# Optimization experiments

Measured on AMD Instinct MI355X. Metric: run time of the kernel, lower is better.

Reference implementation:

```python
import jax, jax.numpy as jnp
import numpy as np

NUM_GRAPHS = 512
NODES_PER_GRAPH = 200  # == N_rois
EDGES_PER_GRAPH = 3200  # avg degree 16
N_ROIS = 200
HIDDEN = 64
OUT = 2


def setup_inputs() -> dict:
    key = jax.random.key(0)
    ks = jax.random.split(key, 7)
    N = NUM_GRAPHS * NODES_PER_GRAPH
    E = NUM_GRAPHS * EDGES_PER_GRAPH
    x = jax.random.normal(ks[0], (N, N_ROIS), dtype=jnp.float32)
    # edges sampled within each graph's node block
    base = jnp.repeat(jnp.arange(NUM_GRAPHS, dtype=jnp.int64) * NODES_PER_GRAPH, EDGES_PER_GRAPH)
    local = jax.random.randint(ks[1], (2, E), 0, NODES_PER_GRAPH, dtype=jnp.int64)
    edge_index = local + base[None, :]
    batch = jnp.arange(N, dtype=jnp.int64) // NODES_PER_GRAPH
    conv_w = jax.random.normal(ks[2], (N_ROIS, HIDDEN), dtype=jnp.float32) * 0.1
    conv_b = jax.random.normal(ks[3], (HIDDEN,), dtype=jnp.float32) * 0.1
    lin_w = jax.random.normal(ks[4], (HIDDEN, OUT), dtype=jnp.float32) * 0.1
    lin_b = jax.random.normal(ks[5], (OUT,), dtype=jnp.float32) * 0.1
    return {"x": x, "edge_index": edge_index, "batch": batch,
            "conv_w": conv_w, "conv_b": conv_b, "lin_w": lin_w, "lin_b": lin_b}


def reference(x, edge_index, batch, conv_w, conv_b, lin_w, lin_b):
    N = x.shape[0]
    # GCNConv: linear transform first (N_rois -> hidden), then normalized aggregation
    h = x @ conv_w  # [N, H]
    loops = jnp.arange(N, dtype=edge_index.dtype)
    src = jnp.concatenate([edge_index[0], loops])  # add self-loops (PyG default)
    dst = jnp.concatenate([edge_index[1], loops])
    deg = jax.ops.segment_sum(jnp.ones_like(dst, dtype=h.dtype), dst, num_segments=N)
    dinv = jnp.where(deg > 0, jax.lax.rsqrt(deg), jnp.zeros_like(deg))
    norm = dinv[src] * dinv[dst]  # D^-1/2 (A+I) D^-1/2 edge weights
    agg = jax.ops.segment_sum(h[src] * norm[:, None], dst, num_segments=N) + conv_b
    hr = jax.nn.relu(agg)
    x_pool = jax.ops.segment_max(hr, batch, num_segments=NUM_GRAPHS)  # [G, H]
    out = x_pool @ lin_w + lin_b  # [G, OUT]
    return out, x_pool
```

## Files before the change

### kernel.cpp

```cpp
#include <hip/hip_runtime.h>

#define NUM_GRAPHS 512
#define NPG 200
#define EPG 3200
#define NROIS 200
#define HID 64
#define OUTC 2
#define APITCH 232
#define HPITCH 232
#define WIMG_ELEMS (7 * 4 * 2 * 64 * 8)
#define WS_NEEDED ((size_t)WIMG_ELEMS * 2)

typedef short v8s __attribute__((ext_vector_type(8)));
typedef float v4f __attribute__((ext_vector_type(4)));

__device__ __forceinline__ unsigned bf16_rne(float f) {
  unsigned u = __float_as_uint(f);
  return (u + 0x7fffu + ((u >> 16) & 1u)) >> 16;
}

__global__ void prep_wimg(const float* __restrict__ cw, unsigned short* __restrict__ wimg) {
  int idx = blockIdx.x * 256 + threadIdx.x;
  if (idx >= WIMG_ELEMS) return;
  int i    = idx & 7;
  int lane = (idx >> 3) & 63;
  int hl   = (idx >> 9) & 1;
  int nt   = (idx >> 10) & 3;
  int kt   = idx >> 12;
  int k  = kt * 32 + (lane >> 4) * 8 + i;
  int ch = nt * 16 + (lane & 15);
  float f = (k < NROIS) ? cw[k * HID + ch] : 0.f;
  unsigned hi = bf16_rne(f);
  float lo = f - __uint_as_float(hi << 16);
  wimg[idx] = hl ? (unsigned short)(__float_as_uint(lo) >> 16) : (unsigned short)hi;
}

struct __align__(16) Smem2 {
  unsigned char adj[208 * APITCH];
  union {
    unsigned short hpTl[HID * HPITCH];
    unsigned int wbuf[2][2048];
  } u;
  int cnt[NPG];
  float dinv[NPG];
  int pool[HID];
};

__device__ __forceinline__ v8s tobf16(const float4& a, const float4& b) {
  v8s r;
  r[0] = (short)bf16_rne(a.x); r[1] = (short)bf16_rne(a.y);
  r[2] = (short)bf16_rne(a.z); r[3] = (short)bf16_rne(a.w);
  r[4] = (short)bf16_rne(b.x); r[5] = (short)bf16_rne(b.y);
  r[6] = (short)bf16_rne(b.z); r[7] = (short)bf16_rne(b.w);
  return r;
}

__device__ __forceinline__ void stageW(Smem2& s, const unsigned short* __restrict__ wimg,
                                       int kt, int buf, int w, int lane) {
  const char* gp = (const char*)wimg + (size_t)kt * 8192 + (size_t)(w * 64 + lane) * 16;
  unsigned char* lp = (unsigned char*)&s.u.wbuf[buf][0] + w * 1024;
  __builtin_amdgcn_global_load_lds(
      (const __attribute__((address_space(1))) unsigned int*)gp,
      (__attribute__((address_space(3))) unsigned int*)lp, 16, 0, 0);
}

__device__ __forceinline__ void xfetch(const float* __restrict__ x, int base,
                                       int kt, int q, const int* mts, const int* nrow,
                                       float4 xa[2][2]) {
  const int k0 = kt * 32 + q * 8;
  const bool ok = (k0 + 8 <= NROIS);
  #pragma unroll
  for (int mi = 0; mi < 2; ++mi) {
    if (mts[mi] >= 0) {
      if (ok) {
        const float* px = x + (size_t)(base + nrow[mi]) * NROIS + k0;
        xa[mi][0] = *(const float4*)px;
        xa[mi][1] = *(const float4*)(px + 4);
      } else {
        xa[mi][0] = make_float4(0.f, 0.f, 0.f, 0.f);
        xa[mi][1] = make_float4(0.f, 0.f, 0.f, 0.f);
      }
    }
  }
}

__global__ __launch_bounds__(512, 4)
void gcn_fused8(const float* __restrict__ x,
                const int* __restrict__ ei,
                const unsigned short* __restrict__ wimg,
                const float* __restrict__ cb,
                const float* __restrict__ lw,
                const float* __restrict__ lb,
                float* __restrict__ out,
                int Etot) {
  __shared__ Smem2 s;
  const int g = blockIdx.x;
  const int tid = threadIdx.x;
  const int base = g * NPG;
  const int ebase = g * EPG;
  const int lane = tid & 63;
  const int w = __builtin_amdgcn_readfirstlane(tid >> 6);
  const int ml = tid & 15;
  const int q  = (tid >> 4) & 3;

  int mts[2];
  mts[0] = w;
  mts[1] = (w < 5) ? 8 + w : -1;
  int nrow[2];
  #pragma unroll
  for (int mi = 0; mi < 2; ++mi) {
    int node = mts[mi] * 16 + ml;
    nrow[mi] = (node < NPG) ? node : 0;
  }

  int esrc[7], edst[7];
  #pragma unroll
  for (int r = 0; r < 7; ++r) {
    int e = tid + r * 512;
    esrc[r] = -1; edst[r] = 0;
    if (e < EPG) {
      esrc[r] = ei[ebase + e] - base;
      edst[r] = ei[Etot + ebase + e] - base;
    }
  }
  float4 xa[2][2];
  xfetch(x, base, 0, q, mts, nrow, xa);
  stageW(s, wimg, 0, 0, w, lane);
  {
    uint4* z = (uint4*)s.adj;
    const uint4 z4 = {0u, 0u, 0u, 0u};
    #pragma unroll
    for (int i = 0; i < 6; ++i) {
      int idx = tid + i * 512;
      if (idx < (208 * APITCH) / 16) z[idx] = z4;
    }
    if (tid < NPG) s.cnt[tid] = 0;
    if (tid < HID) s.pool[tid] = 0;
  }
  __syncthreads();

  {
    unsigned* adjW = (unsigned*)s.adj;
    #pragma unroll
    for (int r = 0; r < 7; ++r) {
      if (esrc[r] >= 0) {
        int idx = edst[r] * APITCH + esrc[r];
        atomicAdd(&adjW[idx >> 2], 1u << ((idx & 3) * 8));
        atomicAdd(&s.cnt[edst[r]], 1);
      }
    }
    if (tid < NPG) {
      int idx = tid * APITCH + tid;
      atomicAdd(&adjW[idx >> 2], 1u << ((idx & 3) * 8));
    }
  }

  v4f acc[2][4];
  #pragma unroll
  for (int a = 0; a < 2; ++a)
    #pragma unroll
    for (int b = 0; b < 4; ++b)
      acc[a][b] = (v4f){0.f, 0.f, 0.f, 0.f};

  for (int kt = 0; kt < 7; ++kt) {
    const int cur = kt & 1;
    if (kt < 6) stageW(s, wimg, kt + 1, cur ^ 1, w, lane);
    v8s xh2[2];
    #pragma unroll
    for (int mi = 0; mi < 2; ++mi)
      if (mts[mi] >= 0) xh2[mi] = tobf16(xa[mi][0], xa[mi][1]);
    if (kt < 6) xfetch(x, base, kt + 1, q, mts, nrow, xa);

    const unsigned short* wb = (const unsigned short*)&s.u.wbuf[cur][0];
    v8s whi[4], wlo[4];
    #pragma unroll
    for (int nt = 0; nt < 4; ++nt) {
      whi[nt] = *(const v8s*)(wb + (size_t)((nt * 2 + 0) * 64 + lane) * 8);
      wlo[nt] = *(const v8s*)(wb + (size_t)((nt * 2 + 1) * 64 + lane) * 8);
    }
    #pragma unroll
    for (int mi = 0; mi < 2; ++mi) {
      if (mts[mi] >= 0) {
        #pragma unroll
        for (int nt = 0; nt < 4; ++nt) {
          acc[mi][nt] = __builtin_amdgcn_mfma_f32_16x16x32_bf16(wlo[nt], xh2[mi], acc[mi][nt], 0, 0, 0);
          acc[mi][nt] = __builtin_amdgcn_mfma_f32_16x16x32_bf16(whi[nt], xh2[mi], acc[mi][nt], 0, 0, 0);
        }
      }
    }
    __syncthreads();
  }

  if (tid < NPG) s.dinv[tid] = rsqrtf((float)(s.cnt[tid] + 1));
  {
    int ch = tid >> 3, grp = tid & 7;
    *(uint2*)&s.u.hpTl[ch * HPITCH + 200 + grp * 4] = (uint2){0u, 0u};
  }
  #pragma unroll
  for (int mi = 0; mi < 2; ++mi) {
    if (mts[mi] >= 0) {
      const int node = mts[mi] * 16 + ml;
      if (node < NPG) {
        const float dv = rsqrtf((float)(s.cnt[node] + 1));
        #pragma unroll
        for (int nt = 0; nt < 4; ++nt) {
          #pragma unroll
          for (int r = 0; r < 4; ++r) {
            const int ch = nt * 16 + q * 4 + r;
            s.u.hpTl[ch * HPITCH + node] = (unsigned short)bf16_rne(dv * acc[mi][nt][r]);
          }
        }
      }
    }
  }
  __syncthreads();

  {
    v4f acc2[2][4];
    #pragma unroll
    for (int a = 0; a < 2; ++a)
      #pragma unroll
      for (int b = 0; b < 4; ++b)
        acc2[a][b] = (v4f){0.f, 0.f, 0.f, 0.f};

    for (int kt = 0; kt < 7; ++kt) {
      const int k0 = kt * 32 + q * 8;

      v8s bf[4];
      #pragma unroll
      for (int nt = 0; nt < 4; ++nt)
        bf[nt] = *(const v8s*)&s.u.hpTl[(nt * 16 + ml) * HPITCH + k0];

      #pragma unroll
      for (int mi = 0; mi < 2; ++mi) {
        if (mts[mi] >= 0) {
          const int row = mts[mi] * 16 + ml;
          const uint2 dd = *(const uint2*)&s.adj[row * APITCH + k0];
          v8s af;
          #pragma unroll
          for (int i = 0; i < 4; ++i) {
            af[i]     = (short)(__float_as_uint((float)((dd.x >> (8 * i)) & 0xffu)) >> 16);
            af[i + 4] = (short)(__float_as_uint((float)((dd.y >> (8 * i)) & 0xffu)) >> 16);
          }
          #pragma unroll
          for (int nt = 0; nt < 4; ++nt)
            acc2[mi][nt] = __builtin_amdgcn_mfma_f32_16x16x32_bf16(af, bf[nt], acc2[mi][nt], 0, 0, 0);
        }
      }
    }

    float cbv[4];
    #pragma unroll
    for (int nt = 0; nt < 4; ++nt) cbv[nt] = cb[nt * 16 + ml];
    float mx[4] = {0.f, 0.f, 0.f, 0.f};
    #pragma unroll
    for (int mi = 0; mi < 2; ++mi) {
      if (mts[mi] >= 0) {
        #pragma unroll
        for (int r = 0; r < 4; ++r) {
          const int row = mts[mi] * 16 + q * 4 + r;
          if (row < NPG) {
            const float dv = s.dinv[row];
            #pragma unroll
            for (int nt = 0; nt < 4; ++nt) {
              float v = fmaxf(fmaf(dv, acc2[mi][nt][r], cbv[nt]), 0.f);
              mx[nt] = fmaxf(mx[nt], v);
            }
          }
        }
      }
    }
    #pragma unroll
    for (int nt = 0; nt < 4; ++nt) {
      mx[nt] = fmaxf(mx[nt], __shfl_xor(mx[nt], 16));
      mx[nt] = fmaxf(mx[nt], __shfl_xor(mx[nt], 32));
    }
    if (q == 0 && (lane >> 5) == 0) {
      #pragma unroll
      for (int nt = 0; nt < 4; ++nt)
        atomicMax(&s.pool[nt * 16 + ml], __float_as_int(mx[nt]));
    }
  }
  __syncthreads();

  if (tid < HID) {
    const float xp = __int_as_float(s.pool[tid]);
    out[NUM_GRAPHS * OUTC + g * HID + tid] = xp;
    float p0 = xp * lw[tid * 2 + 0];
    float p1 = xp * lw[tid * 2 + 1];
    #pragma unroll
    for (int off = 32; off > 0; off >>= 1) {
      p0 += __shfl_down(p0, off);
      p1 += __shfl_down(p1, off);
    }
    if (tid == 0) {
      out[g * OUTC + 0] = p0 + lb[0];
      out[g * OUTC + 1] = p1 + lb[1];
    }
  }
}

struct __align__(16) SmemF {
  unsigned char adj[208 * APITCH];
  unsigned short hpT[HID * HPITCH];
  float dinv[NPG];
  int cnt[NPG];
  int pool[HID];
};

__global__ __launch_bounds__(512, 4)
void gcn_fused_fb(const float* __restrict__ x,
                  const int* __restrict__ ei,
                  const float* __restrict__ cw,
                  const float* __restrict__ cb,
                  const float* __restrict__ lw,
                  const float* __restrict__ lb,
                  float* __restrict__ out,
                  int Etot) {
  __shared__ SmemF s;
  const int g = blockIdx.x;
  const int tid = threadIdx.x;
  const int base = g * NPG;
  const int ebase = g * EPG;
  const int lane = tid & 63;
  const int w = __builtin_amdgcn_readfirstlane(tid >> 6);
  const int ml = tid & 15;
  const int q  = (tid >> 4) & 3;

  {
    uint4* z = (uint4*)&s;
    const uint4 z4 = {0u, 0u, 0u, 0u};
    #pragma unroll
    for (int i = 0; i < 10; ++i) {
      int idx = tid + i * 512;
      if (idx < (208 * APITCH + HID * HPITCH * 2) / 16) z[idx] = z4;
    }
    if (tid < NPG) s.cnt[tid] = 0;
    if (tid < HID) s.pool[tid] = 0;
  }
  __syncthreads();

  int esrc[7], edst[7];
  #pragma unroll
  for (int r = 0; r < 7; ++r) {
    int e = tid + r * 512;
    esrc[r] = -1; edst[r] = 0;
    if (e < EPG) {
      esrc[r] = ei[ebase + e] - base;
      edst[r] = ei[Etot + ebase + e] - base;
      atomicAdd(&s.cnt[edst[r]], 1);
    }
  }
  __syncthreads();

  if (tid < NPG) s.dinv[tid] = rsqrtf((float)(s.cnt[tid] + 1));

  {
    unsigned* adjW = (unsigned*)s.adj;
    #pragma unroll
    for (int r = 0; r < 7; ++r) {
      if (esrc[r] >= 0) {
        int idx = edst[r] * APITCH + esrc[r];
        atomicAdd(&adjW[idx >> 2], 1u << ((idx & 3) * 8));
      }
    }
    if (tid < NPG) {
      int idx = tid * APITCH + tid;
      atomicAdd(&adjW[idx >> 2], 1u << ((idx & 3) * 8));
    }
  }
  __syncthreads();

  {
    int mts[2];
    mts[0] = w;
    mts[1] = (w < 5) ? 8 + w : -1;
    v4f acc[2][4];
    #pragma unroll
    for (int a = 0; a < 2; ++a)
      #pragma unroll
      for (int b = 0; b < 4; ++b)
        acc[a][b] = (v4f){0.f, 0.f, 0.f, 0.f};

    for (int kt = 0; kt < 7; ++kt) {
      const int k0 = kt * 32 + q * 8;
      const bool kok = (k0 < NROIS);
      v8s bhi[4], blo[4];
      #pragma unroll
      for (int nt = 0; nt < 4; ++nt) {
        #pragma unroll
        for (int i = 0; i < 8; ++i) {
          float f = kok ? cw[(k0 + i) * HID + nt * 16 + ml] : 0.f;
          unsigned hb = bf16_rne(f);
          float lo = f - __uint_as_float(hb << 16);
          bhi[nt][i] = (short)hb;
          blo[nt][i] = (short)(__float_as_uint(lo) >> 16);
        }
      }
      #pragma unroll
      for (int mi = 0; mi < 2; ++mi) {
        if (mts[mi] >= 0) {
          const int row = mts[mi] * 16 + ml;
          v8s ahi, alo;
          if (kok && row < NPG) {
            const float* px = x + (size_t)(base + row) * NROIS + k0;
            const float4 f0 = *(const float4*)px;
            const float4 f1 = *(const float4*)(px + 4);
            const float ff[8] = {f0.x, f0.y, f0.z, f0.w, f1.x, f1.y, f1.z, f1.w};
            #pragma unroll
            for (int i = 0; i < 8; ++i) {
              unsigned u = __float_as_uint(ff[i]);
              unsigned hb = u >> 16;
              float lo = ff[i] - __uint_as_float(hb << 16);
              ahi[i] = (short)hb;
              alo[i] = (short)(__float_as_uint(lo) >> 16);
            }
          } else {
            #pragma unroll
            for (int i = 0; i < 8; ++i) { ahi[i] = 0; alo[i] = 0; }
          }
          #pragma unroll
          for (int nt = 0; nt < 4; ++nt) {
            acc[mi][nt] = __builtin_amdgcn_mfma_f32_16x16x32_bf16(ahi, blo[nt], acc[mi][nt], 0, 0, 0);
            acc[mi][nt] = __builtin_amdgcn_mfma_f32_16x16x32_bf16(alo, bhi[nt], acc[mi][nt], 0, 0, 0);
            acc[mi][nt] = __builtin_amdgcn_mfma_f32_16x16x32_bf16(ahi, bhi[nt], acc[mi][nt], 0, 0, 0);
          }
        }
      }
    }
    #pragma unroll
    for (int mi = 0; mi < 2; ++mi) {
      if (mts[mi] >= 0) {
        #pragma unroll
        for (int r = 0; r < 4; ++r) {
          const int row = mts[mi] * 16 + q * 4 + r;
          if (row < NPG) {
            const float dv = s.dinv[row];
            #pragma unroll
            for (int nt = 0; nt < 4; ++nt)
              s.hpT[(nt * 16 + ml) * HPITCH + row] =
                  (unsigned short)bf16_rne(dv * acc[mi][nt][r]);
          }
        }
      }
    }
  }
  __syncthreads();

  {
    int mts[2];
    mts[0] = w;
    mts[1] = (w < 5) ? 8 + w : -1;
    v4f acc2[2][4];
    #pragma unroll
    for (int a = 0; a < 2; ++a)
      #pragma unroll
      for (int b = 0; b < 4; ++b)
        acc2[a][b] = (v4f){0.f, 0.f, 0.f, 0.f};

    for (int kt = 0; kt < 7; ++kt) {
      const int k0 = kt * 32 + q * 8;
      v8s bf[4];
      #pragma unroll
      for (int nt = 0; nt < 4; ++nt)
        bf[nt] = *(const v8s*)&s.hpT[(nt * 16 + ml) * HPITCH + k0];
      #pragma unroll
      for (int mi = 0; mi < 2; ++mi) {
        if (mts[mi] >= 0) {
          const int row = mts[mi] * 16 + ml;
          const uint2 dd = *(const uint2*)&s.adj[row * APITCH + k0];
          v8s af;
          #pragma unroll
          for (int i = 0; i < 4; ++i) {
            af[i]     = (short)(__float_as_uint((float)((dd.x >> (8 * i)) & 0xffu)) >> 16);
            af[i + 4] = (short)(__float_as_uint((float)((dd.y >> (8 * i)) & 0xffu)) >> 16);
          }
          #pragma unroll
          for (int nt = 0; nt < 4; ++nt)
            acc2[mi][nt] = __builtin_amdgcn_mfma_f32_16x16x32_bf16(af, bf[nt], acc2[mi][nt], 0, 0, 0);
        }
      }
    }

    float cbv[4];
    #pragma unroll
    for (int nt = 0; nt < 4; ++nt) cbv[nt] = cb[nt * 16 + ml];
    float mx[4] = {0.f, 0.f, 0.f, 0.f};
    #pragma unroll
    for (int mi = 0; mi < 2; ++mi) {
      if (mts[mi] >= 0) {
        #pragma unroll
        for (int r = 0; r < 4; ++r) {
          const int row = mts[mi] * 16 + q * 4 + r;
          if (row < NPG) {
            const float dv = s.dinv[row];
            #pragma unroll
            for (int nt = 0; nt < 4; ++nt) {
              float v = fmaxf(fmaf(dv, acc2[mi][nt][r], cbv[nt]), 0.f);
              mx[nt] = fmaxf(mx[nt], v);
            }
          }
        }
      }
    }
    #pragma unroll
    for (int nt = 0; nt < 4; ++nt) {
      mx[nt] = fmaxf(mx[nt], __shfl_xor(mx[nt], 16));
      mx[nt] = fmaxf(mx[nt], __shfl_xor(mx[nt], 32));
    }
    if (q == 0 && (lane >> 5) == 0) {
      #pragma unroll
      for (int nt = 0; nt < 4; ++nt)
        atomicMax(&s.pool[nt * 16 + ml], __float_as_int(mx[nt]));
    }
  }
  __syncthreads();

  if (tid < HID) {
    const float xp = __int_as_float(s.pool[tid]);
    out[NUM_GRAPHS * OUTC + g * HID + tid] = xp;
    float p0 = xp * lw[tid * 2 + 0];
    float p1 = xp * lw[tid * 2 + 1];
    #pragma unroll
    for (int off = 32; off > 0; off >>= 1) {
      p0 += __shfl_down(p0, off);
      p1 += __shfl_down(p1, off);
    }
    if (tid == 0) {
      out[g * OUTC + 0] = p0 + lb[0];
      out[g * OUTC + 1] = p1 + lb[1];
    }
  }
}

extern "C" void kernel_launch(void* const* d_in, const int* in_sizes, int n_in,
                              void* d_out, int out_size, void* d_ws, size_t ws_size,
                              hipStream_t stream) {
  const float* x  = (const float*)d_in[0];
  const int*   ei = (const int*)d_in[1];
  const float* cw = (const float*)d_in[3];
  const float* cb = (const float*)d_in[4];
  const float* lw = (const float*)d_in[5];
  const float* lb = (const float*)d_in[6];
  const int Etot = in_sizes[1] / 2;

  if (ws_size >= WS_NEEDED) {
    unsigned short* wimg = (unsigned short*)d_ws;
    prep_wimg<<<(WIMG_ELEMS + 255) / 256, 256, 0, stream>>>(cw, wimg);
    gcn_fused8<<<NUM_GRAPHS, 512, 0, stream>>>(x, ei, wimg, cb, lw, lb,
                                               (float*)d_out, Etot);
  } else {
    gcn_fused_fb<<<NUM_GRAPHS, 512, 0, stream>>>(x, ei, cw, cb, lw, lb,
                                                 (float*)d_out, Etot);
  }
}
```

Baseline: 144.7 us.

## Deepen GEMM prefetch pipeline to multi-stage with manual waitcnt barriers

Replaces the double-buffered K loop of the x@W GEMM with a fully unrolled schedule. It keeps three x register slots and four LDS weight buffers in flight and issues prefetches two steps ahead. Barriers become explicit s_waitcnt vmcnt(N) plus s_barrier pairs, so outstanding loads are not drained every iteration. The adjacency buffer shrinks to 200 rows and out-of-range row reads are clamped. The extra registers and hand-counted vmcnt values risk lower occupancy or subtle correctness issues if load counts differ per wave.

```diff
diff --git a/kernel.cpp b/kernel.cpp
--- a/kernel.cpp
+++ b/kernel.cpp
@@ -36,10 +36,10 @@
 }
 
 struct __align__(16) Smem2 {
-  unsigned char adj[208 * APITCH];
+  unsigned char adj[200 * APITCH];
   union {
     unsigned short hpTl[HID * HPITCH];
-    unsigned int wbuf[2][2048];
+    unsigned int wbuf4[4][2048];
   } u;
   int cnt[NPG];
   float dinv[NPG];
@@ -55,10 +55,10 @@
   return r;
 }
 
-__device__ __forceinline__ void stageW(Smem2& s, const unsigned short* __restrict__ wimg,
-                                       int kt, int buf, int w, int lane) {
-  const char* gp = (const char*)wimg + (size_t)kt * 8192 + (size_t)(w * 64 + lane) * 16;
-  unsigned char* lp = (unsigned char*)&s.u.wbuf[buf][0] + w * 1024;
+__device__ __forceinline__ void stageW4(Smem2& s, const unsigned short* __restrict__ wimg,
+                                        int t, int w, int lane) {
+  const char* gp = (const char*)wimg + (size_t)t * 8192 + (size_t)(w * 64 + lane) * 16;
+  unsigned char* lp = (unsigned char*)&s.u.wbuf4[t & 3][0] + w * 1024;
   __builtin_amdgcn_global_load_lds(
       (const __attribute__((address_space(1))) unsigned int*)gp,
       (__attribute__((address_space(3))) unsigned int*)lp, 16, 0, 0);
@@ -84,8 +84,36 @@
   }
 }
 
+template<int KT, int SL>
+__device__ __forceinline__ void kt_step(Smem2& s, float4 (&xa)[3][2][2],
+                                        v4f (&acc)[2][4], const int* mts, int lane) {
+  v8s xh2[2];
+  #pragma unroll
+  for (int mi = 0; mi < 2; ++mi)
+    if (mts[mi] >= 0) xh2[mi] = tobf16(xa[SL][mi][0], xa[SL][mi][1]);
+  const unsigned short* wb = (const unsigned short*)&s.u.wbuf4[KT & 3][0];
+  v8s whi[4], wlo[4];
+  #pragma unroll
+  for (int nt = 0; nt < 4; ++nt) {
+    whi[nt] = *(const v8s*)(wb + (size_t)((nt * 2 + 0) * 64 + lane) * 8);
+    wlo[nt] = *(const v8s*)(wb + (size_t)((nt * 2 + 1) * 64 + lane) * 8);
+  }
+  #pragma unroll
+  for (int mi = 0; mi < 2; ++mi) {
+    if (mts[mi] >= 0) {
+      #pragma unroll
+      for (int nt = 0; nt < 4; ++nt) {
+        acc[mi][nt] = __builtin_amdgcn_mfma_f32_16x16x32_bf16(wlo[nt], xh2[mi], acc[mi][nt], 0, 0, 0);
+        acc[mi][nt] = __builtin_amdgcn_mfma_f32_16x16x32_bf16(whi[nt], xh2[mi], acc[mi][nt], 0, 0, 0);
+      }
+    }
+  }
+}
+
+#define WAITBAR(N) asm volatile("s_waitcnt vmcnt(" #N ") lgkmcnt(0)\n\ts_barrier" ::: "memory")
+
 __global__ __launch_bounds__(512, 4)
-void gcn_fused8(const float* __restrict__ x,
+void gcn_fused9(const float* __restrict__ x,
                 const int* __restrict__ ei,
                 const unsigned short* __restrict__ wimg,
                 const float* __restrict__ cb,
@@ -113,6 +141,12 @@
     nrow[mi] = (node < NPG) ? node : 0;
   }
 
+  float4 xa[3][2][2];
+  xfetch(x, base, 0, q, mts, nrow, xa[0]);
+  xfetch(x, base, 1, q, mts, nrow, xa[1]);
+  xfetch(x, base, 2, q, mts, nrow, xa[2]);
+  stageW4(s, wimg, 0, w, lane);
+  stageW4(s, wimg, 1, w, lane);
   int esrc[7], edst[7];
   #pragma unroll
   for (int r = 0; r < 7; ++r) {
@@ -123,16 +157,13 @@
       edst[r] = ei[Etot + ebase + e] - base;
     }
   }
-  float4 xa[2][2];
-  xfetch(x, base, 0, q, mts, nrow, xa);
-  stageW(s, wimg, 0, 0, w, lane);
   {
     uint4* z = (uint4*)s.adj;
     const uint4 z4 = {0u, 0u, 0u, 0u};
     #pragma unroll
     for (int i = 0; i < 6; ++i) {
       int idx = tid + i * 512;
-      if (idx < (208 * APITCH) / 16) z[idx] = z4;
+      if (idx < (200 * APITCH) / 16) z[idx] = z4;
     }
     if (tid < NPG) s.cnt[tid] = 0;
     if (tid < HID) s.pool[tid] = 0;
@@ -162,34 +193,29 @@
     for (int b = 0; b < 4; ++b)
       acc[a][b] = (v4f){0.f, 0.f, 0.f, 0.f};
 
-  for (int kt = 0; kt < 7; ++kt) {
-    const int cur = kt & 1;
-    if (kt < 6) stageW(s, wimg, kt + 1, cur ^ 1, w, lane);
-    v8s xh2[2];
-    #pragma unroll
-    for (int mi = 0; mi < 2; ++mi)
-      if (mts[mi] >= 0) xh2[mi] = tobf16(xa[mi][0], xa[mi][1]);
-    if (kt < 6) xfetch(x, base, kt + 1, q, mts, nrow, xa);
-
-    const unsigned short* wb = (const unsigned short*)&s.u.wbuf[cur][0];
-    v8s whi[4], wlo[4];
-    #pragma unroll
-    for (int nt = 0; nt < 4; ++nt) {
-      whi[nt] = *(const v8s*)(wb + (size_t)((nt * 2 + 0) * 64 + lane) * 8);
-      wlo[nt] = *(const v8s*)(wb + (size_t)((nt * 2 + 1) * 64 + lane) * 8);
-    }
-    #pragma unroll
-    for (int mi = 0; mi < 2; ++mi) {
-      if (mts[mi] >= 0) {
-        #pragma unroll
-        for (int nt = 0; nt < 4; ++nt) {
-          acc[mi][nt] = __builtin_amdgcn_mfma_f32_16x16x32_bf16(wlo[nt], xh2[mi], acc[mi][nt], 0, 0, 0);
-          acc[mi][nt] = __builtin_amdgcn_mfma_f32_16x16x32_bf16(whi[nt], xh2[mi], acc[mi][nt], 0, 0, 0);
-        }
-      }
-    }
-    __syncthreads();
-  }
+  stageW4(s, wimg, 2, w, lane);
+  stageW4(s, wimg, 3, w, lane);
+  kt_step<0, 0>(s, xa, acc, mts, lane);
+  kt_step<1, 1>(s, xa, acc, mts, lane);
+  xfetch(x, base, 3, q, mts, nrow, xa[0]);
+  xfetch(x, base, 4, q, mts, nrow, xa[1]);
+  if (w < 5) WAITBAR(8); else WAITBAR(4);
+
+  stageW4(s, wimg, 4, w, lane);
+  stageW4(s, wimg, 5, w, lane);
+  kt_step<2, 2>(s, xa, acc, mts, lane);
+  kt_step<3, 0>(s, xa, acc, mts, lane);
+  xfetch(x, base, 5, q, mts, nrow, xa[2]);
+  xfetch(x, base, 6, q, mts, nrow, xa[0]);
+  if (w < 5) WAITBAR(8); else WAITBAR(4);
+
+  stageW4(s, wimg, 6, w, lane);
+  kt_step<4, 1>(s, xa, acc, mts, lane);
+  kt_step<5, 2>(s, xa, acc, mts, lane);
+  WAITBAR(0);
+
+  kt_step<6, 0>(s, xa, acc, mts, lane);
+  __syncthreads();
 
   if (tid < NPG) s.dinv[tid] = rsqrtf((float)(s.cnt[tid] + 1));
   {
@@ -235,7 +261,8 @@
       for (int mi = 0; mi < 2; ++mi) {
         if (mts[mi] >= 0) {
           const int row = mts[mi] * 16 + ml;
-          const uint2 dd = *(const uint2*)&s.adj[row * APITCH + k0];
+          const int arow = (row < NPG) ? row : 0;
+          const uint2 dd = *(const uint2*)&s.adj[arow * APITCH + k0];
           v8s af;
           #pragma unroll
           for (int i = 0; i < 4; ++i) {
@@ -547,7 +574,7 @@
   if (ws_size >= WS_NEEDED) {
     unsigned short* wimg = (unsigned short*)d_ws;
     prep_wimg<<<(WIMG_ELEMS + 255) / 256, 256, 0, stream>>>(cw, wimg);
-    gcn_fused8<<<NUM_GRAPHS, 512, 0, stream>>>(x, ei, wimg, cb, lw, lb,
+    gcn_fused9<<<NUM_GRAPHS, 512, 0, stream>>>(x, ei, wimg, cb, lw, lb,
                                                (float*)d_out, Etot);
   } else {
     gcn_fused_fb<<<NUM_GRAPHS, 512, 0, stream>>>(x, ei, cw, cb, lw, lb,
```

New measurement: 148.0 us. 1.02x slower.
